# Performance work log

Measured on AMD Instinct MI355X. Metric: run time of the kernel, lower is better.

## Reference

```python
import jax, jax.numpy as jnp
import numpy as np

NUM_REL = 8
NUM_NODE = 100000
TYPED_NUM_NODE = 50000   # typed_num_node per relation (static)
EDGES_PER_REL = 800000   # avg degree 16
IN_C = 128
HID_C = 128


def setup_inputs() -> dict:
    key = jax.random.key(0)
    k1, k2, k3, k4, k5 = jax.random.split(key, 5)
    x = jax.random.normal(k1, (NUM_NODE, IN_C), dtype=jnp.float32)
    rel_weight = jax.random.normal(k2, (NUM_REL, IN_C, HID_C), dtype=jnp.float32) * 0.05
    sub_ptr = jnp.sort(jax.random.randint(k3, (NUM_REL, TYPED_NUM_NODE + 1), 0, EDGES_PER_REL), axis=-1)
    sub_idx = jax.random.randint(k4, (NUM_REL, EDGES_PER_REL), 0, NUM_NODE)
    sub_target = jax.random.randint(k5, (NUM_REL, TYPED_NUM_NODE), 0, NUM_NODE)
    return {"x": x, "rel_weight": rel_weight, "sub_ptr": sub_ptr,
            "sub_idx": sub_idx, "sub_target": sub_target}


def _csr_segment_ids(ptr):
    # CSR ptr [N+1] -> per-edge destination segment id [E]
    e = jnp.arange(EDGES_PER_REL)
    return jnp.clip(jnp.searchsorted(ptr, e, side='right') - 1, 0, TYPED_NUM_NODE - 1)


def reference(x, rel_weight, sub_ptr, sub_idx, sub_target):
    outs = []
    for r in range(NUM_REL):  # small fixed relation count
        seg = _csr_segment_ids(sub_ptr[r])
        # sage_sum_forward: sum neighbor features per destination node
        agg = jax.ops.segment_sum(x[sub_idx[r]], seg, num_segments=TYPED_NUM_NODE)  # [T, C]
        outs.append(agg @ rel_weight[r])  # [T, H]
    arr = jnp.concatenate(outs, axis=0)            # [R*T, H]
    tgt = sub_target.reshape(-1)                   # [R*T]
    out = jnp.zeros((NUM_NODE, HID_C), dtype=x.dtype).at[tgt].add(arr)
    return out
```

## Files before the change

kernel.cpp:

```cpp
#include <hip/hip_runtime.h>

#define NREL 8
#define NNODE 100000
#define TNODE 50000
#define NEDGE 800000
#define C 128
#define TILE_T 64
#define NTILE ((TNODE + TILE_T - 1) / TILE_T)
#define NENT (NREL * TNODE)
#define NB_SCAN ((NNODE + 255) / 256)

typedef unsigned int u32;
typedef unsigned short u16;
typedef __attribute__((ext_vector_type(8))) short bf16x8;
typedef __attribute__((ext_vector_type(4))) float f32x4;

__device__ __forceinline__ float bf2f(u16 h) {
    union { u32 u; float f; } c; c.u = ((u32)h) << 16; return c.f;
}
__device__ __forceinline__ u16 f2bf(float f) {
    union { float f; u32 u; } c; c.f = f;
    u32 u = c.u + 0x7FFFu + ((c.u >> 16) & 1u);
    return (u16)(u >> 16);
}
__device__ __forceinline__ u32 pack2(float a, float b) {
    return (u32)f2bf(a) | ((u32)f2bf(b) << 16);
}
__device__ __forceinline__ float2 unpack_bf2(u32 p) {
    union { u32 u; float f; } a, b;
    a.u = p << 16; b.u = p & 0xFFFF0000u;
    return make_float2(a.f, b.f);
}
__device__ __forceinline__ void fma4(float4& acc, float a, float w0, float w1, float w2, float w3) {
    acc.x = fmaf(a, w0, acc.x);
    acc.y = fmaf(a, w1, acc.y);
    acc.z = fmaf(a, w2, acc.z);
    acc.w = fmaf(a, w3, acc.w);
}
__device__ __forceinline__ void add8(float* a, uint4 v) {
    const float2 f0 = unpack_bf2(v.x), f1 = unpack_bf2(v.y);
    const float2 f2 = unpack_bf2(v.z), f3 = unpack_bf2(v.w);
    a[0] += f0.x; a[1] += f0.y; a[2] += f1.x; a[3] += f1.y;
    a[4] += f2.x; a[5] += f2.y; a[6] += f3.x; a[7] += f3.y;
}

__global__ __launch_bounds__(256)
void convert_x_kernel(const float* __restrict__ x, u16* __restrict__ xb, int n4) {
    int i = blockIdx.x * 256 + threadIdx.x;
    const int stride = gridDim.x * 256;
    for (; i < n4; i += stride) {
        const float4 v = ((const float4*)x)[i];
        ushort4 o;
        o.x = f2bf(v.x); o.y = f2bf(v.y); o.z = f2bf(v.z); o.w = f2bf(v.w);
        ((ushort4*)xb)[i] = o;
    }
}

__global__ __launch_bounds__(256)
void convert_w_kernel(const float* __restrict__ w, u16* __restrict__ wtb) {
    const int o = blockIdx.x * 256 + threadIdx.x;
    if (o < NREL * C * C) {
        const int r = o >> 14, rem = o & 16383, cc = rem >> 7, k = rem & 127;
        wtb[o] = f2bf(w[(r << 14) + k * C + cc]);
    }
}

__global__ __launch_bounds__(256, 6)
void gather_kernel(const u16* __restrict__ xb, const int* __restrict__ ptr,
                   const int* __restrict__ idx, u16* __restrict__ P) {
    const int lane = threadIdx.x & 63;
    const int wid  = threadIdx.x >> 6;
    const int g    = blockIdx.x * 4 + wid;
    const int r    = g / TNODE;
    const int t    = g - r * TNODE;

    const int* pr = ptr + r * (TNODE + 1);
    const int* er = idx + (size_t)r * NEDGE;
    const int start = (t == 0) ? 0 : pr[t];
    const int end   = (t == TNODE - 1) ? NEDGE : pr[t + 1];

    const int q  = lane >> 4;
    const int sl = lane & 15;
    float accA[8], accB[8];
    #pragma unroll
    for (int j = 0; j < 8; ++j) { accA[j] = 0.f; accB[j] = 0.f; }
    const u16* xcol = xb + sl * 8;

    for (int base = start; base < end; base += 64) {
        const int cnt = min(end - base, 64);
        int myi = (lane < cnt) ? er[base + lane] : 0;
        int i = 0;
        for (; i + 8 <= cnt; i += 8) {
            const int sA = __shfl(myi, i + q);
            const int sB = __shfl(myi, i + 4 + q);
            const uint4 vA = *(const uint4*)(xcol + (size_t)sA * C);
            const uint4 vB = *(const uint4*)(xcol + (size_t)sB * C);
            add8(accA, vA);
            add8(accB, vB);
        }
        if (i + 4 <= cnt) {
            const int sA = __shfl(myi, i + q);
            const uint4 vA = *(const uint4*)(xcol + (size_t)sA * C);
            add8(accA, vA);
            i += 4;
        }
        if (i < cnt) {
            const int rem = cnt - i;
            const int sA = __shfl(myi, i + ((q < rem) ? q : 0));
            if (q < rem) {
                const uint4 vA = *(const uint4*)(xcol + (size_t)sA * C);
                add8(accA, vA);
            }
        }
    }
    #pragma unroll
    for (int j = 0; j < 8; ++j) {
        accA[j] += accB[j];
        accA[j] += __shfl_xor(accA[j], 16);
        accA[j] += __shfl_xor(accA[j], 32);
    }
    if (q == 0) {
        uint4 o;
        o.x = pack2(accA[0], accA[1]);
        o.y = pack2(accA[2], accA[3]);
        o.z = pack2(accA[4], accA[5]);
        o.w = pack2(accA[6], accA[7]);
        *(uint4*)(P + (size_t)g * C + sl * 8) = o;
    }
}

__global__ __launch_bounds__(256)
void hist_kernel(const int* __restrict__ tgt, int* __restrict__ count) {
    const int g = blockIdx.x * 256 + threadIdx.x;
    if (g < NENT) atomicAdd(&count[tgt[g]], 1);
}

__global__ __launch_bounds__(256)
void scan1_kernel(const int* __restrict__ count, int* __restrict__ bsum) {
    __shared__ int s[256];
    const int tid = threadIdx.x;
    const int i = blockIdx.x * 256 + tid;
    s[tid] = (i < NNODE) ? count[i] : 0;
    __syncthreads();
    for (int st = 128; st > 0; st >>= 1) {
        if (tid < st) s[tid] += s[tid + st];
        __syncthreads();
    }
    if (tid == 0) bsum[blockIdx.x] = s[0];
}

__global__ __launch_bounds__(512)
void scan2_kernel(int* __restrict__ bsum) {
    __shared__ int s[512];
    const int tid = threadIdx.x;
    const int v = (tid < NB_SCAN) ? bsum[tid] : 0;
    s[tid] = v;
    __syncthreads();
    for (int st = 1; st < 512; st <<= 1) {
        const int t = (tid >= st) ? s[tid - st] : 0;
        __syncthreads();
        s[tid] += t;
        __syncthreads();
    }
    if (tid < NB_SCAN) bsum[tid] = s[tid] - v;
}

__global__ __launch_bounds__(256)
void scan3_kernel(const int* __restrict__ count, const int* __restrict__ bsum,
                  int* __restrict__ offsets, int* __restrict__ cursor) {
    __shared__ int s[256];
    const int tid = threadIdx.x;
    const int i = blockIdx.x * 256 + tid;
    const int v = (i < NNODE) ? count[i] : 0;
    s[tid] = v;
    __syncthreads();
    for (int st = 1; st < 256; st <<= 1) {
        const int t = (tid >= st) ? s[tid - st] : 0;
        __syncthreads();
        s[tid] += t;
        __syncthreads();
    }
    if (i < NNODE) {
        const int off = bsum[blockIdx.x] + s[tid] - v;
        offsets[i] = off;
        cursor[i]  = off;
    }
}

__global__ __launch_bounds__(256)
void fill_kernel(const int* __restrict__ tgt, int* __restrict__ cursor, int* __restrict__ list) {
    const int g = blockIdx.x * 256 + threadIdx.x;
    if (g < NENT) {
        const int pos = atomicAdd(&cursor[tgt[g]], 1);
        list[pos] = g;
    }
}

__global__ __launch_bounds__(256, 3)
void gemm_mfma_kernel(u16* P, const u16* __restrict__ wtb) {
    __shared__ u16 sB[C * 136];
    __shared__ u16 sA[TILE_T * 136];

    const int tid  = threadIdx.x;
    const int tile = blockIdx.x;
    const int r    = blockIdx.y;

    {
        const uint4* src = (const uint4*)(wtb + (size_t)r * C * C);
        #pragma unroll
        for (int i = 0; i < 8; ++i) {
            const int f = tid + i * 256;
            const int col = f >> 4, unit = f & 15;
            *(uint4*)(sB + col * 136 + unit * 8) = src[f];
        }
    }
    {
        #pragma unroll
        for (int i = 0; i < 4; ++i) {
            const int f = tid + i * 256;
            const int row = f >> 4, unit = f & 15;
            const int t = tile * TILE_T + row;
            uint4 v = make_uint4(0u, 0u, 0u, 0u);
            if (t < TNODE)
                v = *(const uint4*)(P + ((size_t)r * TNODE + t) * C + unit * 8);
            *(uint4*)(sA + row * 136 + unit * 8) = v;
        }
    }
    __syncthreads();

    const int lane = tid & 63;
    const int wr   = (tid >> 6) * 16;
    const int fr   = lane & 15;
    const int fq   = lane >> 4;

    f32x4 acc[8];
    #pragma unroll
    for (int cf = 0; cf < 8; ++cf) acc[cf] = (f32x4){0.f, 0.f, 0.f, 0.f};

    #pragma unroll
    for (int ks = 0; ks < 4; ++ks) {
        const bf16x8 a = *(const bf16x8*)(sA + (wr + fr) * 136 + ks * 32 + fq * 8);
        #pragma unroll
        for (int cf = 0; cf < 8; ++cf) {
            const bf16x8 b = *(const bf16x8*)(sB + (cf * 16 + fr) * 136 + ks * 32 + fq * 8);
            acc[cf] = __builtin_amdgcn_mfma_f32_16x16x32_bf16(a, b, acc[cf], 0, 0, 0);
        }
    }

    #pragma unroll
    for (int cf = 0; cf < 8; ++cf) {
        #pragma unroll
        for (int j = 0; j < 4; ++j) {
            const int row = wr + fq * 4 + j;
            sA[row * 136 + cf * 16 + fr] = f2bf(acc[cf][j]);
        }
    }
    __syncthreads();

    #pragma unroll
    for (int i = 0; i < 4; ++i) {
        const int f = tid + i * 256;
        const int row = f >> 4, unit = f & 15;
        const int t = tile * TILE_T + row;
        if (t < TNODE)
            *(uint4*)(P + ((size_t)r * TNODE + t) * C + unit * 8) =
                *(const uint4*)(sA + row * 136 + unit * 8);
    }
}

__global__ __launch_bounds__(256)
void out_gather_kernel(const u16* __restrict__ P, const int* __restrict__ offsets,
                       const int* __restrict__ count, const int* __restrict__ list,
                       float* __restrict__ out) {
    const int lane = threadIdx.x & 63;
    const int n = blockIdx.x * 4 + (threadIdx.x >> 6);
    if (n >= NNODE) return;
    const int st = offsets[n];
    const int en = st + count[n];
    float2 a0 = make_float2(0.f, 0.f), a1 = make_float2(0.f, 0.f);
    int i = st;
    for (; i + 2 <= en; i += 2) {
        const u32 v0 = ((const u32*)(P + (size_t)list[i] * C))[lane];
        const u32 v1 = ((const u32*)(P + (size_t)list[i + 1] * C))[lane];
        const float2 f0 = unpack_bf2(v0), f1 = unpack_bf2(v1);
        a0.x += f0.x; a0.y += f0.y;
        a1.x += f1.x; a1.y += f1.y;
    }
    if (i < en) {
        const float2 f0 = unpack_bf2(((const u32*)(P + (size_t)list[i] * C))[lane]);
        a0.x += f0.x; a0.y += f0.y;
    }
    a0.x += a1.x; a0.y += a1.y;
    ((float2*)(out + (size_t)n * C))[lane] = a0;
}

__device__ __forceinline__ void add4(float4& acc, const float4& b) {
    acc.x += b.x; acc.y += b.y; acc.z += b.z; acc.w += b.w;
}
__global__ __launch_bounds__(256, 1)
void rgcn_fused_kernel(const float* __restrict__ x, const float* __restrict__ w,
                       const int* __restrict__ ptr, const int* __restrict__ idx,
                       const int* __restrict__ tgt, float* __restrict__ out) {
    __shared__ float sW[C * C];
    __shared__ float sAgg[TILE_T][C + 4];
    const int tid = threadIdx.x, tile = blockIdx.x, r = blockIdx.y;
    {
        const float4* src = (const float4*)(w + (size_t)r * C * C);
        float4* dst = (float4*)sW;
        #pragma unroll
        for (int i = 0; i < 16; ++i) dst[tid + i * 256] = src[tid + i * 256];
    }
    {
        const int tl = tid >> 2, g = tid & 3;
        const int t = tile * TILE_T + tl;
        float4 a[8];
        #pragma unroll
        for (int j = 0; j < 8; ++j) a[j] = make_float4(0.f, 0.f, 0.f, 0.f);
        if (t < TNODE) {
            const int* pr = ptr + (size_t)r * (TNODE + 1);
            const int* er = idx + (size_t)r * NEDGE;
            int e = (t == 0) ? 0 : pr[t];
            const int end = (t == TNODE - 1) ? NEDGE : pr[t + 1];
            for (; e < end; ++e) {
                const int s0 = er[e];
                const float4* r0 = (const float4*)(x + (size_t)s0 * C) + g * 8;
                #pragma unroll
                for (int j = 0; j < 8; ++j) add4(a[j], r0[j]);
            }
        }
        float* rowp = &sAgg[tl][g * 32];
        #pragma unroll
        for (int j = 0; j < 8; ++j) ((float4*)rowp)[j] = a[j];
    }
    __syncthreads();
    const int tg = tid >> 4, cg = tid & 15;
    float4 acc0[4], acc1[4];
    #pragma unroll
    for (int i = 0; i < 4; ++i) {
        acc0[i] = make_float4(0.f, 0.f, 0.f, 0.f);
        acc1[i] = make_float4(0.f, 0.f, 0.f, 0.f);
    }
    for (int k4 = 0; k4 < C / 4; ++k4) {
        float4 av[4];
        #pragma unroll
        for (int i = 0; i < 4; ++i) av[i] = *(const float4*)&sAgg[tg * 4 + i][k4 * 4];
        #pragma unroll
        for (int kk = 0; kk < 4; ++kk) {
            const int k = k4 * 4 + kk;
            const float4 w0 = *(const float4*)&sW[k * C + cg * 4];
            const float4 w1 = *(const float4*)&sW[k * C + 64 + cg * 4];
            #pragma unroll
            for (int i = 0; i < 4; ++i) {
                const float a = ((const float*)&av[i])[kk];
                fma4(acc0[i], a, w0.x, w0.y, w0.z, w0.w);
                fma4(acc1[i], a, w1.x, w1.y, w1.z, w1.w);
            }
        }
    }
    const int* tr = tgt + (size_t)r * TNODE;
    #pragma unroll
    for (int i = 0; i < 4; ++i) {
        const int t = tile * TILE_T + tg * 4 + i;
        if (t < TNODE) {
            const int node = tr[t];
            float* ob = out + (size_t)node * C + cg * 4;
            unsafeAtomicAdd(ob + 0, acc0[i].x);  unsafeAtomicAdd(ob + 1, acc0[i].y);
            unsafeAtomicAdd(ob + 2, acc0[i].z);  unsafeAtomicAdd(ob + 3, acc0[i].w);
            unsafeAtomicAdd(ob + 64, acc1[i].x); unsafeAtomicAdd(ob + 65, acc1[i].y);
            unsafeAtomicAdd(ob + 66, acc1[i].z); unsafeAtomicAdd(ob + 67, acc1[i].w);
        }
    }
}

extern "C" void kernel_launch(void* const* d_in, const int* in_sizes, int n_in,
                              void* d_out, int out_size, void* d_ws, size_t ws_size,
                              hipStream_t stream) {
    const float* x   = (const float*)d_in[0];
    const float* w   = (const float*)d_in[1];
    const int*   ptr = (const int*)d_in[2];
    const int*   idx = (const int*)d_in[3];
    const int*   tgt = (const int*)d_in[4];
    float* out = (float*)d_out;

    const size_t P_OFF    = 0;
    const size_t XB_OFF   = 104000000;
    const size_t WTB_OFF  = 130000000;
    const size_t CNT_OFF  = 131000000;
    const size_t OFFS_OFF = 131500000;
    const size_t CUR_OFF  = 132000000;
    const size_t BSUM_OFF = 132500000;
    const size_t LIST_OFF = 133000000;
    const size_t WS_NEED  = 135000000;

    if (ws_size >= WS_NEED) {
        char* base = (char*)d_ws;
        u16*   P       = (u16*)(base + P_OFF);
        u16*   xb      = (u16*)(base + XB_OFF);
        u16*   wtb     = (u16*)(base + WTB_OFF);
        int*   count   = (int*)(base + CNT_OFF);
        int*   offsets = (int*)(base + OFFS_OFF);
        int*   cursor  = (int*)(base + CUR_OFF);
        int*   bsum    = (int*)(base + BSUM_OFF);
        int*   list    = (int*)(base + LIST_OFF);

        convert_x_kernel<<<2048, 256, 0, stream>>>(x, xb, NNODE * C / 4);
        convert_w_kernel<<<(NREL * C * C + 255) / 256, 256, 0, stream>>>(w, wtb);

        gather_kernel<<<NENT / 4, 256, 0, stream>>>(xb, ptr, idx, P);

        hipMemsetAsync(count, 0, NNODE * sizeof(int), stream);
        hist_kernel<<<(NENT + 255) / 256, 256, 0, stream>>>(tgt, count);
        scan1_kernel<<<NB_SCAN, 256, 0, stream>>>(count, bsum);
        scan2_kernel<<<1, 512, 0, stream>>>(bsum);
        scan3_kernel<<<NB_SCAN, 256, 0, stream>>>(count, bsum, offsets, cursor);
        fill_kernel<<<(NENT + 255) / 256, 256, 0, stream>>>(tgt, cursor, list);

        dim3 grid(NTILE, NREL);
        gemm_mfma_kernel<<<grid, 256, 0, stream>>>(P, wtb);

        out_gather_kernel<<<(NNODE + 3) / 4, 256, 0, stream>>>(P, offsets, count, list, out);
    } else {
        hipMemsetAsync(out, 0, (size_t)NNODE * C * sizeof(float), stream);
        dim3 grid(NTILE, NREL);
        rgcn_fused_kernel<<<grid, 256, 0, stream>>>(x, w, ptr, idx, tgt, out);
    }
}
```

Baseline: 356.4 us.

## Fuse neighbor gather into MFMA GEMM kernel via shared-memory staging

Merges the separate gather kernel and the GEMM kernel into one kernel. Each 512-thread block gathers and sums neighbor rows for its 64 target nodes directly into the shared-memory A tile, then runs the bf16 MFMA GEMM and writes P once. This removes the round trip of the aggregated P tensor through global memory and one kernel launch. It also switches the accumulators to packed float2 adds. In exchange, each block has fewer waves per node and uses more LDS, and the GEMM stage must wait for the slowest gather wave in the block.

```diff
diff --git a/kernel.cpp b/kernel.cpp
--- a/kernel.cpp
+++ b/kernel.cpp
@@ -14,6 +14,7 @@
 typedef unsigned short u16;
 typedef __attribute__((ext_vector_type(8))) short bf16x8;
 typedef __attribute__((ext_vector_type(4))) float f32x4;
+typedef __attribute__((ext_vector_type(2))) float f32x2;
 
 __device__ __forceinline__ float bf2f(u16 h) {
     union { u32 u; float f; } c; c.u = ((u32)h) << 16; return c.f;
@@ -30,18 +31,21 @@
     union { u32 u; float f; } a, b;
     a.u = p << 16; b.u = p & 0xFFFF0000u;
     return make_float2(a.f, b.f);
+}
+__device__ __forceinline__ f32x2 bits2(u32 p) {
+    union { u32 u[2]; f32x2 f; } c;
+    c.u[0] = p << 16; c.u[1] = p & 0xFFFF0000u;
+    return c.f;
+}
+__device__ __forceinline__ void addp(f32x2* a, uint4 v) {
+    a[0] += bits2(v.x); a[1] += bits2(v.y);
+    a[2] += bits2(v.z); a[3] += bits2(v.w);
 }
 __device__ __forceinline__ void fma4(float4& acc, float a, float w0, float w1, float w2, float w3) {
     acc.x = fmaf(a, w0, acc.x);
     acc.y = fmaf(a, w1, acc.y);
     acc.z = fmaf(a, w2, acc.z);
     acc.w = fmaf(a, w3, acc.w);
-}
-__device__ __forceinline__ void add8(float* a, uint4 v) {
-    const float2 f0 = unpack_bf2(v.x), f1 = unpack_bf2(v.y);
-    const float2 f2 = unpack_bf2(v.z), f3 = unpack_bf2(v.w);
-    a[0] += f0.x; a[1] += f0.y; a[2] += f1.x; a[3] += f1.y;
-    a[4] += f2.x; a[5] += f2.y; a[6] += f3.x; a[7] += f3.y;
 }
 
 __global__ __launch_bounds__(256)
@@ -65,70 +69,6 @@
     }
 }
 
-__global__ __launch_bounds__(256, 6)
-void gather_kernel(const u16* __restrict__ xb, const int* __restrict__ ptr,
-                   const int* __restrict__ idx, u16* __restrict__ P) {
-    const int lane = threadIdx.x & 63;
-    const int wid  = threadIdx.x >> 6;
-    const int g    = blockIdx.x * 4 + wid;
-    const int r    = g / TNODE;
-    const int t    = g - r * TNODE;
-
-    const int* pr = ptr + r * (TNODE + 1);
-    const int* er = idx + (size_t)r * NEDGE;
-    const int start = (t == 0) ? 0 : pr[t];
-    const int end   = (t == TNODE - 1) ? NEDGE : pr[t + 1];
-
-    const int q  = lane >> 4;
-    const int sl = lane & 15;
-    float accA[8], accB[8];
-    #pragma unroll
-    for (int j = 0; j < 8; ++j) { accA[j] = 0.f; accB[j] = 0.f; }
-    const u16* xcol = xb + sl * 8;
-
-    for (int base = start; base < end; base += 64) {
-        const int cnt = min(end - base, 64);
-        int myi = (lane < cnt) ? er[base + lane] : 0;
-        int i = 0;
-        for (; i + 8 <= cnt; i += 8) {
-            const int sA = __shfl(myi, i + q);
-            const int sB = __shfl(myi, i + 4 + q);
-            const uint4 vA = *(const uint4*)(xcol + (size_t)sA * C);
-            const uint4 vB = *(const uint4*)(xcol + (size_t)sB * C);
-            add8(accA, vA);
-            add8(accB, vB);
-        }
-        if (i + 4 <= cnt) {
-            const int sA = __shfl(myi, i + q);
-            const uint4 vA = *(const uint4*)(xcol + (size_t)sA * C);
-            add8(accA, vA);
-            i += 4;
-        }
-        if (i < cnt) {
-            const int rem = cnt - i;
-            const int sA = __shfl(myi, i + ((q < rem) ? q : 0));
-            if (q < rem) {
-                const uint4 vA = *(const uint4*)(xcol + (size_t)sA * C);
-                add8(accA, vA);
-            }
-        }
-    }
-    #pragma unroll
-    for (int j = 0; j < 8; ++j) {
-        accA[j] += accB[j];
-        accA[j] += __shfl_xor(accA[j], 16);
-        accA[j] += __shfl_xor(accA[j], 32);
-    }
-    if (q == 0) {
-        uint4 o;
-        o.x = pack2(accA[0], accA[1]);
-        o.y = pack2(accA[2], accA[3]);
-        o.z = pack2(accA[4], accA[5]);
-        o.w = pack2(accA[6], accA[7]);
-        *(uint4*)(P + (size_t)g * C + sl * 8) = o;
-    }
-}
-
 __global__ __launch_bounds__(256)
 void hist_kernel(const int* __restrict__ tgt, int* __restrict__ count) {
     const int g = blockIdx.x * 256 + threadIdx.x;
@@ -196,70 +136,126 @@
     }
 }
 
-__global__ __launch_bounds__(256, 3)
-void gemm_mfma_kernel(u16* P, const u16* __restrict__ wtb) {
+__global__ __launch_bounds__(512, 6)
+void fused_gather_gemm_kernel(const u16* __restrict__ xb, const int* __restrict__ ptr,
+                              const int* __restrict__ idx, const u16* __restrict__ wtb,
+                              u16* __restrict__ P) {
     __shared__ u16 sB[C * 136];
     __shared__ u16 sA[TILE_T * 136];
 
     const int tid  = threadIdx.x;
     const int tile = blockIdx.x;
     const int r    = blockIdx.y;
+    const int w    = tid >> 6;
+    const int lane = tid & 63;
 
     {
         const uint4* src = (const uint4*)(wtb + (size_t)r * C * C);
         #pragma unroll
-        for (int i = 0; i < 8; ++i) {
-            const int f = tid + i * 256;
+        for (int i = 0; i < 4; ++i) {
+            const int f = tid + i * 512;
             const int col = f >> 4, unit = f & 15;
             *(uint4*)(sB + col * 136 + unit * 8) = src[f];
         }
     }
-    {
-        #pragma unroll
-        for (int i = 0; i < 4; ++i) {
-            const int f = tid + i * 256;
-            const int row = f >> 4, unit = f & 15;
-            const int t = tile * TILE_T + row;
-            uint4 v = make_uint4(0u, 0u, 0u, 0u);
-            if (t < TNODE)
-                v = *(const uint4*)(P + ((size_t)r * TNODE + t) * C + unit * 8);
-            *(uint4*)(sA + row * 136 + unit * 8) = v;
-        }
-    }
-    __syncthreads();
-
-    const int lane = tid & 63;
-    const int wr   = (tid >> 6) * 16;
-    const int fr   = lane & 15;
-    const int fq   = lane >> 4;
-
-    f32x4 acc[8];
-    #pragma unroll
-    for (int cf = 0; cf < 8; ++cf) acc[cf] = (f32x4){0.f, 0.f, 0.f, 0.f};
+
+    const int* pr = ptr + r * (TNODE + 1);
+    const int* er = idx + (size_t)r * NEDGE;
+    const int q  = lane >> 4;
+    const int sl = lane & 15;
+    const u16* xcol = xb + sl * 8;
+
+    for (int s = 0; s < 8; ++s) {
+        const int tl = w * 8 + s;
+        const int t  = tile * TILE_T + tl;
+        f32x2 accA[4], accB[4];
+        #pragma unroll
+        for (int j = 0; j < 4; ++j) { accA[j] = (f32x2){0.f, 0.f}; accB[j] = (f32x2){0.f, 0.f}; }
+
+        if (t < TNODE) {
+            const int start = (t == 0) ? 0 : pr[t];
+            const int end   = (t == TNODE - 1) ? NEDGE : pr[t + 1];
+
+            for (int base = start; base < end; base += 64) {
+                const int cnt = min(end - base, 64);
+                int myi = (lane < cnt) ? er[base + lane] : 0;
+                int i = 0;
+                for (; i + 8 <= cnt; i += 8) {
+                    const int sA0 = __shfl(myi, i + q);
+                    const int sB0 = __shfl(myi, i + 4 + q);
+                    const uint4 vA = *(const uint4*)(xcol + (size_t)sA0 * C);
+                    const uint4 vB = *(const uint4*)(xcol + (size_t)sB0 * C);
+                    addp(accA, vA);
+                    addp(accB, vB);
+                }
+                if (i + 4 <= cnt) {
+                    const int sA0 = __shfl(myi, i + q);
+                    const uint4 vA = *(const uint4*)(xcol + (size_t)sA0 * C);
+                    addp(accA, vA);
+                    i += 4;
+                }
+                if (i < cnt) {
+                    const int rem = cnt - i;
+                    const int sA0 = __shfl(myi, i + ((q < rem) ? q : 0));
+                    if (q < rem) {
+                        const uint4 vA = *(const uint4*)(xcol + (size_t)sA0 * C);
+                        addp(accA, vA);
+                    }
+                }
+            }
+        }
+        #pragma unroll
+        for (int j = 0; j < 4; ++j) {
+            accA[j] += accB[j];
+            accA[j].x += __shfl_xor(accA[j].x, 16);
+            accA[j].y += __shfl_xor(accA[j].y, 16);
+            accA[j].x += __shfl_xor(accA[j].x, 32);
+            accA[j].y += __shfl_xor(accA[j].y, 32);
+        }
+        if (q == 0) {
+            uint4 o;
+            o.x = pack2(accA[0].x, accA[0].y);
+            o.y = pack2(accA[1].x, accA[1].y);
+            o.z = pack2(accA[2].x, accA[2].y);
+            o.w = pack2(accA[3].x, accA[3].y);
+            *(uint4*)(sA + tl * 136 + sl * 8) = o;
+        }
+    }
+    __syncthreads();
+
+    const int wr    = (w & 3) * 16;
+    const int cbase = (w >> 2) * 4;
+    const int fr    = lane & 15;
+    const int fq    = lane >> 4;
+
+    f32x4 acc[4];
+    #pragma unroll
+    for (int cf = 0; cf < 4; ++cf) acc[cf] = (f32x4){0.f, 0.f, 0.f, 0.f};
 
     #pragma unroll
     for (int ks = 0; ks < 4; ++ks) {
         const bf16x8 a = *(const bf16x8*)(sA + (wr + fr) * 136 + ks * 32 + fq * 8);
         #pragma unroll
-        for (int cf = 0; cf < 8; ++cf) {
-            const bf16x8 b = *(const bf16x8*)(sB + (cf * 16 + fr) * 136 + ks * 32 + fq * 8);
+        for (int cf = 0; cf < 4; ++cf) {
+            const bf16x8 b = *(const bf16x8*)(sB + ((cbase + cf) * 16 + fr) * 136 + ks * 32 + fq * 8);
             acc[cf] = __builtin_amdgcn_mfma_f32_16x16x32_bf16(a, b, acc[cf], 0, 0, 0);
         }
     }
-
-    #pragma unroll
-    for (int cf = 0; cf < 8; ++cf) {
+    __syncthreads();
+
+    #pragma unroll
+    for (int cf = 0; cf < 4; ++cf) {
         #pragma unroll
         for (int j = 0; j < 4; ++j) {
             const int row = wr + fq * 4 + j;
-            sA[row * 136 + cf * 16 + fr] = f2bf(acc[cf][j]);
-        }
-    }
-    __syncthreads();
-
-    #pragma unroll
-    for (int i = 0; i < 4; ++i) {
-        const int f = tid + i * 256;
+            sA[row * 136 + (cbase + cf) * 16 + fr] = f2bf(acc[cf][j]);
+        }
+    }
+    __syncthreads();
+
+    #pragma unroll
+    for (int i = 0; i < 2; ++i) {
+        const int f = tid + i * 512;
         const int row = f >> 4, unit = f & 15;
         const int t = tile * TILE_T + row;
         if (t < TNODE)
@@ -406,8 +402,6 @@
         convert_x_kernel<<<2048, 256, 0, stream>>>(x, xb, NNODE * C / 4);
         convert_w_kernel<<<(NREL * C * C + 255) / 256, 256, 0, stream>>>(w, wtb);
 
-        gather_kernel<<<NENT / 4, 256, 0, stream>>>(xb, ptr, idx, P);
-
         hipMemsetAsync(count, 0, NNODE * sizeof(int), stream);
         hist_kernel<<<(NENT + 255) / 256, 256, 0, stream>>>(tgt, count);
         scan1_kernel<<<NB_SCAN, 256, 0, stream>>>(count, bsum);
@@ -416,7 +410,7 @@
         fill_kernel<<<(NENT + 255) / 256, 256, 0, stream>>>(tgt, cursor, list);
 
         dim3 grid(NTILE, NREL);
-        gemm_mfma_kernel<<<grid, 256, 0, stream>>>(P, wtb);
+        fused_gather_gemm_kernel<<<grid, 512, 0, stream>>>(xb, ptr, idx, wtb, P);
 
         out_gather_kernel<<<(NNODE + 3) / 4, 256, 0, stream>>>(P, offsets, count, list, out);
     } else {
```

Result: no change. 351.5 us (-1.4%).
